# Kernel optimization log

Hardware: AMD Instinct MI355X
Metric: run time of the kernel (lower is better)

Reference implementation:

```python
import math
import jax, jax.numpy as jnp
import numpy as np
from jax import lax

MUL = 16           # multiplicity of 0e and 1o in input and output irreps
NRB = 8            # num_radial_basis
DIAMETER = 3.0
STEPS = (1.0, 1.0, 1.0)
DIM = 4 * MUL      # 16 scalars + 16 vectors * 3 = 64 channels


def _constants():
    # lattice from __init__: arange(-s, s+1) * step per axis, s = floor(r/step)
    r = DIAMETER / 2
    axes = [np.arange(-math.floor(r / st), math.floor(r / st) + 1.0) * st for st in STEPS]
    lattice = np.stack(np.meshgrid(*axes, indexing='ij'), axis=-1)  # [Kx,Ky,Kz,3]
    d = np.linalg.norm(lattice, axis=-1)                            # [Kx,Ky,Kz]
    # soft_one_hot_linspace(basis='smooth_finite', cutoff=True)
    values = np.linspace(0.0, r, NRB + 2)[1:-1]
    step = values[1] - values[0]
    diff = (d[..., None] - values) / step
    inside = diff ** 2 < 1.0
    emb = np.where(inside, 1.14136 * np.exp(2.0) * np.exp(-2.0 / np.where(inside, 1.0 - diff ** 2, 1.0)), 0.0)
    # spherical harmonics, normalize=True, normalization='component'
    n = lattice / np.maximum(d[..., None], 1e-12)  # unit vectors; 0 at the origin voxel
    sh0 = np.ones_like(d)                          # Y_0 (component normalized)
    sh1 = np.sqrt(3.0) * n                         # Y_1 (component normalized)
    return emb.astype(np.float32), sh0.astype(np.float32), sh1.astype(np.float32)

EMB, SH0, SH1 = _constants()
KX, KY, KZ = SH0.shape  # 3,3,3


def setup_inputs() -> dict:
    key = jax.random.key(0)
    ks = jax.random.split(key, 7)
    B, G = 4, 32
    return {
        'x': jax.random.normal(ks[0], (B, G, G, G, DIM), jnp.float32),
        'W_sc0': jax.random.normal(ks[1], (MUL, MUL), jnp.float32),  # Linear 0e->0e
        'W_sc1': jax.random.normal(ks[2], (MUL, MUL), jnp.float32),  # Linear 1o->1o
        'w1': jax.random.normal(ks[3], (NRB, MUL, MUL), jnp.float32),  # path 0e x 0e -> 0e
        'w2': jax.random.normal(ks[4], (NRB, MUL, MUL), jnp.float32),  # path 0e x 1o -> 1o
        'w3': jax.random.normal(ks[5], (NRB, MUL, MUL), jnp.float32),  # path 1o x 0e -> 1o
        'w4': jax.random.normal(ks[6], (NRB, MUL, MUL), jnp.float32),  # path 1o x 1o -> 0e
    }


def _kernel(w1, w2, w3, w4):
    # radial basis -> per-voxel path weights, divided by kernel volume (as in source)
    emb, sh0, sh1 = jnp.asarray(EMB), jnp.asarray(SH0), jnp.asarray(SH1)
    norm = float(KX * KY * KZ)
    W1, W2, W3, W4 = [jnp.einsum('xyzk,kio->xyzio', emb, w) / norm for w in (w1, w2, w3, w4)]
    # path normalization: each output irrep receives 2 paths of fan_in mul*1 = 16 -> 1/sqrt(32)
    alpha = 1.0 / np.sqrt(2.0 * MUL)
    # tp.right blocks (Clebsch-Gordan contractions, lmax=1):
    k00 = alpha * W1 * sh0[..., None, None]                                              # [.,i,o]
    k01 = alpha * jnp.einsum('xyzio,xyzm->xyziom', W2, sh1).reshape(KX, KY, KZ, MUL, 3 * MUL)
    k10 = (alpha / np.sqrt(3.0)) * jnp.einsum('xyzio,xyzm->xyzimo', W4, sh1).reshape(KX, KY, KZ, 3 * MUL, MUL)
    k11 = alpha * jnp.einsum('xyzio,mn->xyzimon', W3 * sh0[..., None, None],
                             jnp.eye(3, dtype=W3.dtype)).reshape(KX, KY, KZ, 3 * MUL, 3 * MUL)
    return jnp.concatenate([jnp.concatenate([k00, k01], axis=-1),
                            jnp.concatenate([k10, k11], axis=-1)], axis=-2)  # [Kx,Ky,Kz,64,64]


def reference(x, W_sc0, W_sc1, w1, w2, w3, w4):
    B, X, Y, Z, _ = x.shape
    inv_sqrt_mul = 1.0 / np.sqrt(MUL)
    # self-connection: e3nn Linear per irrep (applied pointwise over b,x,y,z)
    xs = x[..., :MUL]                                   # [B,X,Y,Z,16] scalars
    xv = x[..., MUL:].reshape(B, X, Y, Z, MUL, 3)       # [B,X,Y,Z,16,3] vectors
    sc_s = (xs @ W_sc0) * inv_sqrt_mul
    sc_v = jnp.einsum('bxyzic,io->bxyzoc', xv, W_sc1) * inv_sqrt_mul
    sc = jnp.concatenate([sc_s, sc_v.reshape(B, X, Y, Z, 3 * MUL)], axis=-1)
    # position-dependent equivariant kernel + standard 3D conv
    k = _kernel(w1, w2, w3, w4)
    conv = lax.conv_general_dilated(x, k, (1, 1, 1), 'SAME',
                                    dimension_numbers=('NXYZC', 'XYZIO', 'NXYZC'))
    return sc + conv
```

## Files before the change

kernel.cpp:

```cpp
#include <hip/hip_runtime.h>

typedef unsigned short u16;
typedef unsigned int u32;
typedef __bf16 bf16x8 __attribute__((ext_vector_type(8)));
typedef float f32x4 __attribute__((ext_vector_type(4)));
typedef u32 u32x4 __attribute__((ext_vector_type(4)));

#define AS1 __attribute__((address_space(1)))
#define AS3 __attribute__((address_space(3)))

__device__ __align__(16) u16 g_kT[27 * 64 * 64];
__device__ __align__(16) u16 g_kTr[27 * 8 * 512];

__device__ __forceinline__ u16 f2bf(float f) {
    unsigned int u = __float_as_uint(f);
    u += 0x7FFFu + ((u >> 16) & 1u);
    return (u16)(u >> 16);
}

__device__ __forceinline__ u32 pack_bf(float a, float b) {
    u32 ua = __float_as_uint(a) + 0x8000u;
    u32 ub = __float_as_uint(b) + 0x8000u;
    return __builtin_amdgcn_perm(ub, ua, 0x07060302u);
}

__global__ __launch_bounds__(64) void build_k(
    const float* __restrict__ Wsc0, const float* __restrict__ Wsc1,
    const float* __restrict__ w1, const float* __restrict__ w2,
    const float* __restrict__ w3, const float* __restrict__ w4)
{
    const int t = blockIdx.x;
    const int c = threadIdx.x;
    const int dx = t / 9 - 1, dy = (t / 3) % 3 - 1, dz = t % 3 - 1;
    const float d = sqrtf((float)(dx * dx + dy * dy + dz * dz));
    const float step = 1.5f / 9.0f;
    float emb[8];
#pragma unroll
    for (int k = 0; k < 8; ++k) {
        float diff = (d - (float)(k + 1) * step) / step;
        float q = diff * diff;
        emb[k] = (q < 1.0f) ? 1.14136f * expf(2.0f - 2.0f / (1.0f - q)) : 0.0f;
    }
    const float dn = fmaxf(d, 1e-12f);
    const float s3 = 1.7320508075688772f;
    const float sh1[3] = { s3 * (float)dx / dn, s3 * (float)dy / dn, s3 * (float)dz / dn };
    const float alpha  = 0.17677669529663687f;
    const float alpha3 = alpha * 0.57735026918962576f;

    u16* outp = &g_kT[(t * 64 + c) * 64];
    const int base2 = ((t * 2 + (c >> 5)) * 2 + ((c >> 4) & 1)) * 2;
    const int l15c  = c & 15;
    auto put = [&](int r, float v) {
        u16 h = f2bf(v);
        outp[r] = h;
        g_kTr[(base2 + (r >> 5)) * 512 + (((r >> 3) & 3) * 16 + l15c) * 8 + (r & 7)] = h;
    };

    if (c < 16) {
        const int o = c;
#pragma unroll
        for (int i = 0; i < 16; ++i) {
            float W1 = 0.f, W4 = 0.f;
#pragma unroll
            for (int k = 0; k < 8; ++k) {
                W1 += emb[k] * w1[k * 256 + i * 16 + o];
                W4 += emb[k] * w4[k * 256 + i * 16 + o];
            }
            W1 *= (1.0f / 27.0f); W4 *= (1.0f / 27.0f);
            float v0 = alpha * W1;
            if (t == 13) v0 += 0.25f * Wsc0[i * 16 + o];
            put(i, v0);
            const float base = alpha3 * W4;
#pragma unroll
            for (int m = 0; m < 3; ++m) put(16 + 3 * i + m, base * sh1[m]);
        }
    } else {
        const int o = (c - 16) / 3, nc = (c - 16) % 3;
#pragma unroll
        for (int i = 0; i < 16; ++i) {
            float W2 = 0.f, W3 = 0.f;
#pragma unroll
            for (int k = 0; k < 8; ++k) {
                W2 += emb[k] * w2[k * 256 + i * 16 + o];
                W3 += emb[k] * w3[k * 256 + i * 16 + o];
            }
            W2 *= (1.0f / 27.0f); W3 *= (1.0f / 27.0f);
            put(i, alpha * W2 * sh1[nc]);
#pragma unroll
            for (int m = 0; m < 3; ++m) {
                float v = (m == nc) ? alpha * W3 : 0.0f;
                if (t == 13 && m == nc) v += 0.25f * Wsc1[i * 16 + o];
                put(16 + 3 * i + m, v);
            }
        }
    }
}

__global__ __launch_bounds__(256) void cvt_x(
    const float* __restrict__ x, u16* __restrict__ xb, u32* __restrict__ zp)
{
    const int tid = threadIdx.x;
    if (blockIdx.x == 0) {
        u32x4 z = {0u, 0u, 0u, 0u};
        *reinterpret_cast<u32x4*>(zp + tid * 4) = z;
    }
    const size_t base = ((size_t)blockIdx.x * 256 + tid) * 8;
    const float4* s = reinterpret_cast<const float4*>(x + base);
    float4 v0 = s[0], v1 = s[1];
    u32x4 p;
    p[0] = pack_bf(v0.x, v0.y); p[1] = pack_bf(v0.z, v0.w);
    p[2] = pack_bf(v1.x, v1.y); p[3] = pack_bf(v1.z, v1.w);
    *reinterpret_cast<u32x4*>(xb + base) = p;
}

#define NROWS4 612
#define NCHUNK 77
#define LDSB   (NCHUNK * 1024)

#define ISSUE_B(s, t) \
  { const char* _p = bTr + (t) * 8192; \
    asm volatile("global_load_dwordx4 %0, %4, off\n\t" \
                 "global_load_dwordx4 %1, %4, off offset:1024\n\t" \
                 "global_load_dwordx4 %2, %4, off offset:2048\n\t" \
                 "global_load_dwordx4 %3, %4, off offset:3072" \
                 : "=&v"(B##s##0), "=&v"(B##s##1), "=&v"(B##s##2), "=&v"(B##s##3) \
                 : "v"(_p)); }

#define LOADA2(s, i0, i1, RCC) { \
  const int _r  = rbase + (RCC); \
  const int _o0 = _r * 128 + ((kg ^ (_r & 7)) << 4); \
  A##s##i0 = *reinterpret_cast<const bf16x8*>(abase + _o0); \
  A##s##i1 = *reinterpret_cast<const bf16x8*>(abase + (_o0 ^ 64)); }

#define RCC4(T, YY, MT) ((((T)/9)*6 + (YY) + (((T)/3)%3))*34 + ((T)%3) + (MT)*16)

#define LOAD_A8(s, T) \
  LOADA2(s, 0, 1, RCC4(T,0,0)) \
  LOADA2(s, 2, 3, RCC4(T,0,1)) \
  LOADA2(s, 4, 5, RCC4(T,1,0)) \
  LOADA2(s, 6, 7, RCC4(T,1,1))

#define WAITV(N) \
  asm volatile("s_waitcnt vmcnt(" #N ")" ::: "memory"); \
  __builtin_amdgcn_sched_barrier(0);

#define BC(x) __builtin_bit_cast(bf16x8, x)

#define MFMA16(bs, as) \
  acc000 = __builtin_amdgcn_mfma_f32_16x16x32_bf16(BC(B##bs##0), A##as##0, acc000, 0,0,0); \
  acc001 = __builtin_amdgcn_mfma_f32_16x16x32_bf16(BC(B##bs##2), A##as##0, acc001, 0,0,0); \
  acc010 = __builtin_amdgcn_mfma_f32_16x16x32_bf16(BC(B##bs##0), A##as##2, acc010, 0,0,0); \
  acc011 = __builtin_amdgcn_mfma_f32_16x16x32_bf16(BC(B##bs##2), A##as##2, acc011, 0,0,0); \
  acc100 = __builtin_amdgcn_mfma_f32_16x16x32_bf16(BC(B##bs##0), A##as##4, acc100, 0,0,0); \
  acc101 = __builtin_amdgcn_mfma_f32_16x16x32_bf16(BC(B##bs##2), A##as##4, acc101, 0,0,0); \
  acc110 = __builtin_amdgcn_mfma_f32_16x16x32_bf16(BC(B##bs##0), A##as##6, acc110, 0,0,0); \
  acc111 = __builtin_amdgcn_mfma_f32_16x16x32_bf16(BC(B##bs##2), A##as##6, acc111, 0,0,0); \
  acc000 = __builtin_amdgcn_mfma_f32_16x16x32_bf16(BC(B##bs##1), A##as##1, acc000, 0,0,0); \
  acc001 = __builtin_amdgcn_mfma_f32_16x16x32_bf16(BC(B##bs##3), A##as##1, acc001, 0,0,0); \
  acc010 = __builtin_amdgcn_mfma_f32_16x16x32_bf16(BC(B##bs##1), A##as##3, acc010, 0,0,0); \
  acc011 = __builtin_amdgcn_mfma_f32_16x16x32_bf16(BC(B##bs##3), A##as##3, acc011, 0,0,0); \
  acc100 = __builtin_amdgcn_mfma_f32_16x16x32_bf16(BC(B##bs##1), A##as##5, acc100, 0,0,0); \
  acc101 = __builtin_amdgcn_mfma_f32_16x16x32_bf16(BC(B##bs##3), A##as##5, acc101, 0,0,0); \
  acc110 = __builtin_amdgcn_mfma_f32_16x16x32_bf16(BC(B##bs##1), A##as##7, acc110, 0,0,0); \
  acc111 = __builtin_amdgcn_mfma_f32_16x16x32_bf16(BC(B##bs##3), A##as##7, acc111, 0,0,0);

__global__ __launch_bounds__(256, 2) void conv_mfma4(
    const u16* __restrict__ xb, const u32* __restrict__ zp,
    float* __restrict__ out)
{
    extern __shared__ u16 xt[];

    const int bid0 = blockIdx.x;
    const int bid  = (bid0 & 7) * 128 + (bid0 >> 3);
    const int b    = bid >> 8;
    const int X    = (bid >> 3) & 31;
    const int y0   = (bid & 7) << 2;
    const int tid  = threadIdx.x;
    const int wv   = tid >> 6;
    const int lane = tid & 63;
    const int l15  = lane & 15;
    const int kg   = lane >> 4;
    const int yh   = wv >> 1;
    const int nh   = wv & 1;

    const char* bTr = (const char*)g_kTr + nh * 4096 + lane * 16;

    u32x4 B00, B01, B02, B03, B10, B11, B12, B13, B20, B21, B22, B23;
    bf16x8 A00, A01, A02, A03, A04, A05, A06, A07;
    bf16x8 A10, A11, A12, A13, A14, A15, A16, A17;

    ISSUE_B(0, 1)
    ISSUE_B(1, 3)

    {
        const int rloc = lane >> 3;
        const int swz  = (lane & 7) ^ rloc;
#pragma unroll
        for (int i = 0; i < 20; ++i) {
            const int c = wv + i * 4;
            if (c < NCHUNK) {
                const int row = c * 8 + rloc;
                const int dxx = row / 204;
                const int rem = row - dxx * 204;
                const int yi  = rem / 34;
                const int zid = rem - yi * 34;
                const int xin = X + dxx - 1;
                const int yin = y0 + yi - 1;
                const int zin = zid - 1;
                const bool inb = (row < NROWS4) & ((unsigned)xin < 32u)
                               & ((unsigned)yin < 32u) & ((unsigned)zin < 32u);
                const u16* src = inb
                    ? xb + ((size_t)(((b * 32 + xin) * 32 + yin) * 32 + zin) * 64 + swz * 8)
                    : (const u16*)zp;
                __builtin_amdgcn_global_load_lds((const AS1 u32*)src,
                                                 (AS3 u32*)&xt[c * 512], 16, 0, 0);
            }
        }
    }
    asm volatile("s_waitcnt vmcnt(0)" ::: "memory");
    __syncthreads();

    const char* abase = reinterpret_cast<const char*>(xt);
    const int rbase = yh * 68 + l15;

    const f32x4 z4 = {0.f, 0.f, 0.f, 0.f};
    f32x4 acc000 = z4, acc001 = z4, acc010 = z4, acc011 = z4;
    f32x4 acc100 = z4, acc101 = z4, acc110 = z4, acc111 = z4;

    LOAD_A8(0, 1)

    ISSUE_B(2, 4)   LOAD_A8(1, 3)   WAITV(8)  MFMA16(0, 0)
    ISSUE_B(0, 5)   LOAD_A8(0, 4)   WAITV(8)  MFMA16(1, 1)
    ISSUE_B(1, 7)   LOAD_A8(1, 5)   WAITV(8)  MFMA16(2, 0)
    ISSUE_B(2, 9)   LOAD_A8(0, 7)   WAITV(8)  MFMA16(0, 1)
    ISSUE_B(0, 10)  LOAD_A8(1, 9)   WAITV(8)  MFMA16(1, 0)
    ISSUE_B(1, 11)  LOAD_A8(0, 10)  WAITV(8)  MFMA16(2, 1)
    ISSUE_B(2, 12)  LOAD_A8(1, 11)  WAITV(8)  MFMA16(0, 0)
    ISSUE_B(0, 13)  LOAD_A8(0, 12)  WAITV(8)  MFMA16(1, 1)
    ISSUE_B(1, 14)  LOAD_A8(1, 13)  WAITV(8)  MFMA16(2, 0)
    ISSUE_B(2, 15)  LOAD_A8(0, 14)  WAITV(8)  MFMA16(0, 1)
    ISSUE_B(0, 16)  LOAD_A8(1, 15)  WAITV(8)  MFMA16(1, 0)
    ISSUE_B(1, 17)  LOAD_A8(0, 16)  WAITV(8)  MFMA16(2, 1)
    ISSUE_B(2, 19)  LOAD_A8(1, 17)  WAITV(8)  MFMA16(0, 0)
    ISSUE_B(0, 21)  LOAD_A8(0, 19)  WAITV(8)  MFMA16(1, 1)
    ISSUE_B(1, 22)  LOAD_A8(1, 21)  WAITV(8)  MFMA16(2, 0)
    ISSUE_B(2, 23)  LOAD_A8(0, 22)  WAITV(8)  MFMA16(0, 1)
    ISSUE_B(0, 25)  LOAD_A8(1, 23)  WAITV(8)  MFMA16(1, 0)
                    LOAD_A8(0, 25)  WAITV(4)  MFMA16(2, 1)
                                    WAITV(0)  MFMA16(0, 0)

    float* obase = out + (((size_t)(b * 32 + X) * 32 + (y0 + yh * 2)) * 32) * 64
                 + nh * 32 + kg * 4;
    *reinterpret_cast<f32x4*>(obase + l15 * 64)               = acc000;
    *reinterpret_cast<f32x4*>(obase + l15 * 64 + 16)          = acc001;
    *reinterpret_cast<f32x4*>(obase + (16 + l15) * 64)        = acc010;
    *reinterpret_cast<f32x4*>(obase + (16 + l15) * 64 + 16)   = acc011;
    *reinterpret_cast<f32x4*>(obase + 2048 + l15 * 64)        = acc100;
    *reinterpret_cast<f32x4*>(obase + 2048 + l15 * 64 + 16)   = acc101;
    *reinterpret_cast<f32x4*>(obase + 2048 + (16 + l15) * 64) = acc110;
    *reinterpret_cast<f32x4*>(obase + 2048 + (16 + l15) * 64 + 16) = acc111;
}

#define ZS 68
#define NROWS 408

__global__ __launch_bounds__(256, 2) void conv_mfma_fb(
    const float* __restrict__ x, float* __restrict__ out)
{
    __shared__ __align__(16) u16 xts[NROWS * ZS];
    const int bid0 = blockIdx.x;
    const int bid  = (bid0 & 7) * 256 + (bid0 >> 3);
    const int b   = bid >> 9;
    const int X   = (bid >> 4) & 31;
    const int y0  = (bid & 15) << 1;
    const int tid = threadIdx.x;

    {
        const int pr = tid >> 2;
        const int q  = tid & 3;
#pragma unroll
        for (int pass = 0; pass < 7; ++pass) {
            const int idx = pass * 64 + pr;
            if (idx < NROWS) {
                const int rid = idx / 34;
                const int zid = idx - rid * 34;
                const int xin = X + (rid >> 2) - 1;
                const int yin = y0 + (rid & 3) - 1;
                const int zin = zid - 1;
                u32x4 p0 = {0u,0u,0u,0u}, p1 = {0u,0u,0u,0u};
                if ((unsigned)xin < 32u && (unsigned)yin < 32u && (unsigned)zin < 32u) {
                    const float4* src = reinterpret_cast<const float4*>(
                        x + ((((b * 32 + xin) * 32 + yin) * 32 + zin) * 64 + q * 16));
                    float4 v0 = src[0], v1 = src[1], v2 = src[2], v3 = src[3];
                    p0[0] = pack_bf(v0.x, v0.y); p0[1] = pack_bf(v0.z, v0.w);
                    p0[2] = pack_bf(v1.x, v1.y); p0[3] = pack_bf(v1.z, v1.w);
                    p1[0] = pack_bf(v2.x, v2.y); p1[1] = pack_bf(v2.z, v2.w);
                    p1[2] = pack_bf(v3.x, v3.y); p1[3] = pack_bf(v3.z, v3.w);
                }
                u16* dst = &xts[idx * ZS + q * 16];
                *reinterpret_cast<u32x4*>(dst)     = p0;
                *reinterpret_cast<u32x4*>(dst + 8) = p1;
            }
        }
    }
    __syncthreads();

    const int w    = tid >> 6;
    const int lane = tid & 63;
    const int l15  = lane & 15;
    const int kg   = lane >> 4;
    const int mh   = w >> 1;
    const int nh   = w & 1;
    const int chb  = kg * 8;

    const u16* abase = &xts[l15 * ZS + chb];
    const u16* bbase = &g_kT[(nh * 32 + l15) * 64 + chb];

    const f32x4 z4 = {0.f, 0.f, 0.f, 0.f};
    f32x4 acc[2][2] = {{z4, z4}, {z4, z4}};

    constexpr int NT = 19;
    constexpr int TAPS[NT] = {1,3,4,5,7,9,10,11,12,13,14,15,16,17,19,21,22,23,25};

#pragma unroll
    for (int ti = 0; ti < NT; ++ti) {
        const int t = TAPS[ti];
        const int dxt = t / 9, dyt = (t / 3) % 3, dzt = t % 3;
        const int rid = dxt * 4 + mh + dyt;
        bf16x8 bfr[4], afr[4];
#pragma unroll
        for (int kb = 0; kb < 2; ++kb)
#pragma unroll
        for (int nt = 0; nt < 2; ++nt)
            bfr[kb*2+nt] = *reinterpret_cast<const bf16x8*>(
                bbase + (t * 64 + nt * 16) * 64 + kb * 32);
#pragma unroll
        for (int kb = 0; kb < 2; ++kb)
#pragma unroll
        for (int mt = 0; mt < 2; ++mt)
            afr[kb*2+mt] = *reinterpret_cast<const bf16x8*>(
                abase + (rid * 34 + dzt + mt * 16) * ZS + kb * 32);
#pragma unroll
        for (int kb = 0; kb < 2; ++kb)
#pragma unroll
        for (int mt = 0; mt < 2; ++mt)
#pragma unroll
        for (int nt = 0; nt < 2; ++nt)
            acc[mt][nt] = __builtin_amdgcn_mfma_f32_16x16x32_bf16(
                bfr[kb*2+nt], afr[kb*2+mt], acc[mt][nt], 0, 0, 0);
    }

    float* obase = out + (((b * 32 + X) * 32 + (y0 + mh)) * 32) * 64 + nh * 32 + kg * 4;
#pragma unroll
    for (int mt = 0; mt < 2; ++mt)
#pragma unroll
        for (int nt = 0; nt < 2; ++nt) {
            float4 v;
            v.x = acc[mt][nt][0]; v.y = acc[mt][nt][1];
            v.z = acc[mt][nt][2]; v.w = acc[mt][nt][3];
            *reinterpret_cast<float4*>(obase + (mt * 16 + l15) * 64 + nt * 16) = v;
        }
}

extern "C" void kernel_launch(void* const* d_in, const int* in_sizes, int n_in,
                              void* d_out, int out_size, void* d_ws, size_t ws_size,
                              hipStream_t stream)
{
    const float* x    = (const float*)d_in[0];
    const float* Wsc0 = (const float*)d_in[1];
    const float* Wsc1 = (const float*)d_in[2];
    const float* w1   = (const float*)d_in[3];
    const float* w2   = (const float*)d_in[4];
    const float* w3   = (const float*)d_in[5];
    const float* w4   = (const float*)d_in[6];
    float* out = (float*)d_out;

    build_k<<<dim3(27), dim3(64), 0, stream>>>(Wsc0, Wsc1, w1, w2, w3, w4);

    const size_t xb_bytes = (size_t)4 * 32 * 32 * 32 * 64 * 2;
    if (ws_size >= 4096 + xb_bytes) {
        u32* zp = (u32*)d_ws;
        u16* xb = (u16*)((char*)d_ws + 4096);
        cvt_x<<<dim3(4096), dim3(256), 0, stream>>>(x, xb, zp);
        conv_mfma4<<<dim3(1024), dim3(256), LDSB, stream>>>(xb, zp, out);
    } else {
        conv_mfma_fb<<<dim3(2048), dim3(256), 0, stream>>>(x, out);
    }
}
```

Measured before the change: 56.78 us.

## Double per-block Y tile to 8 rows to cut halo reloads

The conv kernel now handles 8 y-rows per block instead of 4, so the LDS input tile grows to 10x34 rows per x-slice (128 KiB) and each wave keeps 16 accumulators instead of 8. The grid shrinks to 512 blocks and occupancy drops to one block per CU. The goal is to reuse each kernel-weight B fragment and each haloed input row over more outputs, which lowers global/L2 traffic and the share of halo loads. In exchange it raises register pressure, leaves fewer blocks than a 256-CU GPU can hold two of, and gives less latency hiding.

New measurement: 57.25 us. No clear change (+0.8%).

```diff
diff --git a/kernel.cpp b/kernel.cpp
--- a/kernel.cpp
+++ b/kernel.cpp
@@ -113,9 +113,9 @@
     *reinterpret_cast<u32x4*>(xb + base) = p;
 }
 
-#define NROWS4 612
-#define NCHUNK 77
-#define LDSB   (NCHUNK * 1024)
+#define NROWS5 1020
+#define NCHUNK5 128
+#define LDSB   (NCHUNK5 * 1024)
 
 #define ISSUE_B(s, t) \
   { const char* _p = bTr + (t) * 8192; \
@@ -129,52 +129,57 @@
 #define LOADA2(s, i0, i1, RCC) { \
   const int _r  = rbase + (RCC); \
   const int _o0 = _r * 128 + ((kg ^ (_r & 7)) << 4); \
-  A##s##i0 = *reinterpret_cast<const bf16x8*>(abase + _o0); \
-  A##s##i1 = *reinterpret_cast<const bf16x8*>(abase + (_o0 ^ 64)); }
-
-#define RCC4(T, YY, MT) ((((T)/9)*6 + (YY) + (((T)/3)%3))*34 + ((T)%3) + (MT)*16)
-
-#define LOAD_A8(s, T) \
-  LOADA2(s, 0, 1, RCC4(T,0,0)) \
-  LOADA2(s, 2, 3, RCC4(T,0,1)) \
-  LOADA2(s, 4, 5, RCC4(T,1,0)) \
-  LOADA2(s, 6, 7, RCC4(T,1,1))
+  A##s##_##i0 = *reinterpret_cast<const bf16x8*>(abase + _o0); \
+  A##s##_##i1 = *reinterpret_cast<const bf16x8*>(abase + (_o0 ^ 64)); }
+
+#define RCC5(T, YY, MT) ((((T)/9)*340 + ((((T)/3)%3) + (YY))*34 + ((T)%3) + (MT)*16))
+
+#define LOAD_A16(s, T) \
+  LOADA2(s, 0,  1,  RCC5(T,0,0)) \
+  LOADA2(s, 2,  3,  RCC5(T,0,1)) \
+  LOADA2(s, 4,  5,  RCC5(T,1,0)) \
+  LOADA2(s, 6,  7,  RCC5(T,1,1)) \
+  LOADA2(s, 8,  9,  RCC5(T,2,0)) \
+  LOADA2(s, 10, 11, RCC5(T,2,1)) \
+  LOADA2(s, 12, 13, RCC5(T,3,0)) \
+  LOADA2(s, 14, 15, RCC5(T,3,1))
 
 #define WAITV(N) \
   asm volatile("s_waitcnt vmcnt(" #N ")" ::: "memory"); \
   __builtin_amdgcn_sched_barrier(0);
 
 #define BC(x) __builtin_bit_cast(bf16x8, x)
-
-#define MFMA16(bs, as) \
-  acc000 = __builtin_amdgcn_mfma_f32_16x16x32_bf16(BC(B##bs##0), A##as##0, acc000, 0,0,0); \
-  acc001 = __builtin_amdgcn_mfma_f32_16x16x32_bf16(BC(B##bs##2), A##as##0, acc001, 0,0,0); \
-  acc010 = __builtin_amdgcn_mfma_f32_16x16x32_bf16(BC(B##bs##0), A##as##2, acc010, 0,0,0); \
-  acc011 = __builtin_amdgcn_mfma_f32_16x16x32_bf16(BC(B##bs##2), A##as##2, acc011, 0,0,0); \
-  acc100 = __builtin_amdgcn_mfma_f32_16x16x32_bf16(BC(B##bs##0), A##as##4, acc100, 0,0,0); \
-  acc101 = __builtin_amdgcn_mfma_f32_16x16x32_bf16(BC(B##bs##2), A##as##4, acc101, 0,0,0); \
-  acc110 = __builtin_amdgcn_mfma_f32_16x16x32_bf16(BC(B##bs##0), A##as##6, acc110, 0,0,0); \
-  acc111 = __builtin_amdgcn_mfma_f32_16x16x32_bf16(BC(B##bs##2), A##as##6, acc111, 0,0,0); \
-  acc000 = __builtin_amdgcn_mfma_f32_16x16x32_bf16(BC(B##bs##1), A##as##1, acc000, 0,0,0); \
-  acc001 = __builtin_amdgcn_mfma_f32_16x16x32_bf16(BC(B##bs##3), A##as##1, acc001, 0,0,0); \
-  acc010 = __builtin_amdgcn_mfma_f32_16x16x32_bf16(BC(B##bs##1), A##as##3, acc010, 0,0,0); \
-  acc011 = __builtin_amdgcn_mfma_f32_16x16x32_bf16(BC(B##bs##3), A##as##3, acc011, 0,0,0); \
-  acc100 = __builtin_amdgcn_mfma_f32_16x16x32_bf16(BC(B##bs##1), A##as##5, acc100, 0,0,0); \
-  acc101 = __builtin_amdgcn_mfma_f32_16x16x32_bf16(BC(B##bs##3), A##as##5, acc101, 0,0,0); \
-  acc110 = __builtin_amdgcn_mfma_f32_16x16x32_bf16(BC(B##bs##1), A##as##7, acc110, 0,0,0); \
-  acc111 = __builtin_amdgcn_mfma_f32_16x16x32_bf16(BC(B##bs##3), A##as##7, acc111, 0,0,0);
-
-__global__ __launch_bounds__(256, 2) void conv_mfma4(
+#define MF(b_, a_, c_) __builtin_amdgcn_mfma_f32_16x16x32_bf16(BC(b_), a_, c_, 0, 0, 0)
+
+#define MFMA32(bs, as) \
+  acc000 = MF(B##bs##0, A##as##_0,  acc000);  acc001 = MF(B##bs##2, A##as##_0,  acc001); \
+  acc010 = MF(B##bs##0, A##as##_2,  acc010);  acc011 = MF(B##bs##2, A##as##_2,  acc011); \
+  acc100 = MF(B##bs##0, A##as##_4,  acc100);  acc101 = MF(B##bs##2, A##as##_4,  acc101); \
+  acc110 = MF(B##bs##0, A##as##_6,  acc110);  acc111 = MF(B##bs##2, A##as##_6,  acc111); \
+  acc200 = MF(B##bs##0, A##as##_8,  acc200);  acc201 = MF(B##bs##2, A##as##_8,  acc201); \
+  acc210 = MF(B##bs##0, A##as##_10, acc210);  acc211 = MF(B##bs##2, A##as##_10, acc211); \
+  acc300 = MF(B##bs##0, A##as##_12, acc300);  acc301 = MF(B##bs##2, A##as##_12, acc301); \
+  acc310 = MF(B##bs##0, A##as##_14, acc310);  acc311 = MF(B##bs##2, A##as##_14, acc311); \
+  acc000 = MF(B##bs##1, A##as##_1,  acc000);  acc001 = MF(B##bs##3, A##as##_1,  acc001); \
+  acc010 = MF(B##bs##1, A##as##_3,  acc010);  acc011 = MF(B##bs##3, A##as##_3,  acc011); \
+  acc100 = MF(B##bs##1, A##as##_5,  acc100);  acc101 = MF(B##bs##3, A##as##_5,  acc101); \
+  acc110 = MF(B##bs##1, A##as##_7,  acc110);  acc111 = MF(B##bs##3, A##as##_7,  acc111); \
+  acc200 = MF(B##bs##1, A##as##_9,  acc200);  acc201 = MF(B##bs##3, A##as##_9,  acc201); \
+  acc210 = MF(B##bs##1, A##as##_11, acc210);  acc211 = MF(B##bs##3, A##as##_11, acc211); \
+  acc300 = MF(B##bs##1, A##as##_13, acc300);  acc301 = MF(B##bs##3, A##as##_13, acc301); \
+  acc310 = MF(B##bs##1, A##as##_15, acc310);  acc311 = MF(B##bs##3, A##as##_15, acc311);
+
+__global__ __launch_bounds__(256, 1) void conv_mfma5(
     const u16* __restrict__ xb, const u32* __restrict__ zp,
     float* __restrict__ out)
 {
     extern __shared__ u16 xt[];
 
     const int bid0 = blockIdx.x;
-    const int bid  = (bid0 & 7) * 128 + (bid0 >> 3);
-    const int b    = bid >> 8;
-    const int X    = (bid >> 3) & 31;
-    const int y0   = (bid & 7) << 2;
+    const int bid  = (bid0 & 7) * 64 + (bid0 >> 3);
+    const int b    = bid >> 7;
+    const int X    = (bid >> 2) & 31;
+    const int y0   = (bid & 3) << 3;
     const int tid  = threadIdx.x;
     const int wv   = tid >> 6;
     const int lane = tid & 63;
@@ -186,8 +191,10 @@
     const char* bTr = (const char*)g_kTr + nh * 4096 + lane * 16;
 
     u32x4 B00, B01, B02, B03, B10, B11, B12, B13, B20, B21, B22, B23;
-    bf16x8 A00, A01, A02, A03, A04, A05, A06, A07;
-    bf16x8 A10, A11, A12, A13, A14, A15, A16, A17;
+    bf16x8 A0_0, A0_1, A0_2,  A0_3,  A0_4,  A0_5,  A0_6,  A0_7,
+           A0_8, A0_9, A0_10, A0_11, A0_12, A0_13, A0_14, A0_15;
+    bf16x8 A1_0, A1_1, A1_2,  A1_3,  A1_4,  A1_5,  A1_6,  A1_7,
+           A1_8, A1_9, A1_10, A1_11, A1_12, A1_13, A1_14, A1_15;
 
     ISSUE_B(0, 1)
     ISSUE_B(1, 3)
@@ -196,69 +203,77 @@
         const int rloc = lane >> 3;
         const int swz  = (lane & 7) ^ rloc;
 #pragma unroll
-        for (int i = 0; i < 20; ++i) {
-            const int c = wv + i * 4;
-            if (c < NCHUNK) {
-                const int row = c * 8 + rloc;
-                const int dxx = row / 204;
-                const int rem = row - dxx * 204;
-                const int yi  = rem / 34;
-                const int zid = rem - yi * 34;
-                const int xin = X + dxx - 1;
-                const int yin = y0 + yi - 1;
-                const int zin = zid - 1;
-                const bool inb = (row < NROWS4) & ((unsigned)xin < 32u)
-                               & ((unsigned)yin < 32u) & ((unsigned)zin < 32u);
-                const u16* src = inb
-                    ? xb + ((size_t)(((b * 32 + xin) * 32 + yin) * 32 + zin) * 64 + swz * 8)
-                    : (const u16*)zp;
-                __builtin_amdgcn_global_load_lds((const AS1 u32*)src,
-                                                 (AS3 u32*)&xt[c * 512], 16, 0, 0);
-            }
+        for (int i = 0; i < 32; ++i) {
+            const int c = wv * 32 + i;
+            const int row = c * 8 + rloc;
+            const int dxx = row / 340;
+            const int rem = row - dxx * 340;
+            const int yi  = rem / 34;
+            const int zid = rem - yi * 34;
+            const int xin = X + dxx - 1;
+            const int yin = y0 + yi - 1;
+            const int zin = zid - 1;
+            const bool inb = (row < NROWS5) & ((unsigned)xin < 32u)
+                           & ((unsigned)yin < 32u) & ((unsigned)zin < 32u);
+            const u16* src = inb
+                ? xb + ((size_t)(((b * 32 + xin) * 32 + yin) * 32 + zin) * 64 + swz * 8)
+                : (const u16*)zp;
+            __builtin_amdgcn_global_load_lds((const AS1 u32*)src,
+                                             (AS3 u32*)&xt[c * 512], 16, 0, 0);
         }
     }
     asm volatile("s_waitcnt vmcnt(0)" ::: "memory");
     __syncthreads();
 
     const char* abase = reinterpret_cast<const char*>(xt);
-    const int rbase = yh * 68 + l15;
+    const int rbase = yh * 136 + l15;
 
     const f32x4 z4 = {0.f, 0.f, 0.f, 0.f};
     f32x4 acc000 = z4, acc001 = z4, acc010 = z4, acc011 = z4;
     f32x4 acc100 = z4, acc101 = z4, acc110 = z4, acc111 = z4;
-
-    LOAD_A8(0, 1)
-
-    ISSUE_B(2, 4)   LOAD_A8(1, 3)   WAITV(8)  MFMA16(0, 0)
-    ISSUE_B(0, 5)   LOAD_A8(0, 4)   WAITV(8)  MFMA16(1, 1)
-    ISSUE_B(1, 7)   LOAD_A8(1, 5)   WAITV(8)  MFMA16(2, 0)
-    ISSUE_B(2, 9)   LOAD_A8(0, 7)   WAITV(8)  MFMA16(0, 1)
-    ISSUE_B(0, 10)  LOAD_A8(1, 9)   WAITV(8)  MFMA16(1, 0)
-    ISSUE_B(1, 11)  LOAD_A8(0, 10)  WAITV(8)  MFMA16(2, 1)
-    ISSUE_B(2, 12)  LOAD_A8(1, 11)  WAITV(8)  MFMA16(0, 0)
-    ISSUE_B(0, 13)  LOAD_A8(0, 12)  WAITV(8)  MFMA16(1, 1)
-    ISSUE_B(1, 14)  LOAD_A8(1, 13)  WAITV(8)  MFMA16(2, 0)
-    ISSUE_B(2, 15)  LOAD_A8(0, 14)  WAITV(8)  MFMA16(0, 1)
-    ISSUE_B(0, 16)  LOAD_A8(1, 15)  WAITV(8)  MFMA16(1, 0)
-    ISSUE_B(1, 17)  LOAD_A8(0, 16)  WAITV(8)  MFMA16(2, 1)
-    ISSUE_B(2, 19)  LOAD_A8(1, 17)  WAITV(8)  MFMA16(0, 0)
-    ISSUE_B(0, 21)  LOAD_A8(0, 19)  WAITV(8)  MFMA16(1, 1)
-    ISSUE_B(1, 22)  LOAD_A8(1, 21)  WAITV(8)  MFMA16(2, 0)
-    ISSUE_B(2, 23)  LOAD_A8(0, 22)  WAITV(8)  MFMA16(0, 1)
-    ISSUE_B(0, 25)  LOAD_A8(1, 23)  WAITV(8)  MFMA16(1, 0)
-                    LOAD_A8(0, 25)  WAITV(4)  MFMA16(2, 1)
-                                    WAITV(0)  MFMA16(0, 0)
-
-    float* obase = out + (((size_t)(b * 32 + X) * 32 + (y0 + yh * 2)) * 32) * 64
+    f32x4 acc200 = z4, acc201 = z4, acc210 = z4, acc211 = z4;
+    f32x4 acc300 = z4, acc301 = z4, acc310 = z4, acc311 = z4;
+
+    LOAD_A16(0, 1)
+
+    ISSUE_B(2, 4)   LOAD_A16(1, 3)   WAITV(8)  MFMA32(0, 0)
+    ISSUE_B(0, 5)   LOAD_A16(0, 4)   WAITV(8)  MFMA32(1, 1)
+    ISSUE_B(1, 7)   LOAD_A16(1, 5)   WAITV(8)  MFMA32(2, 0)
+    ISSUE_B(2, 9)   LOAD_A16(0, 7)   WAITV(8)  MFMA32(0, 1)
+    ISSUE_B(0, 10)  LOAD_A16(1, 9)   WAITV(8)  MFMA32(1, 0)
+    ISSUE_B(1, 11)  LOAD_A16(0, 10)  WAITV(8)  MFMA32(2, 1)
+    ISSUE_B(2, 12)  LOAD_A16(1, 11)  WAITV(8)  MFMA32(0, 0)
+    ISSUE_B(0, 13)  LOAD_A16(0, 12)  WAITV(8)  MFMA32(1, 1)
+    ISSUE_B(1, 14)  LOAD_A16(1, 13)  WAITV(8)  MFMA32(2, 0)
+    ISSUE_B(2, 15)  LOAD_A16(0, 14)  WAITV(8)  MFMA32(0, 1)
+    ISSUE_B(0, 16)  LOAD_A16(1, 15)  WAITV(8)  MFMA32(1, 0)
+    ISSUE_B(1, 17)  LOAD_A16(0, 16)  WAITV(8)  MFMA32(2, 1)
+    ISSUE_B(2, 19)  LOAD_A16(1, 17)  WAITV(8)  MFMA32(0, 0)
+    ISSUE_B(0, 21)  LOAD_A16(0, 19)  WAITV(8)  MFMA32(1, 1)
+    ISSUE_B(1, 22)  LOAD_A16(1, 21)  WAITV(8)  MFMA32(2, 0)
+    ISSUE_B(2, 23)  LOAD_A16(0, 22)  WAITV(8)  MFMA32(0, 1)
+    ISSUE_B(0, 25)  LOAD_A16(1, 23)  WAITV(8)  MFMA32(1, 0)
+                    LOAD_A16(0, 25)  WAITV(4)  MFMA32(2, 1)
+                                     WAITV(0)  MFMA32(0, 0)
+
+    float* obase = out + (((size_t)(b * 32 + X) * 32 + (y0 + yh * 4)) * 32) * 64
                  + nh * 32 + kg * 4;
-    *reinterpret_cast<f32x4*>(obase + l15 * 64)               = acc000;
-    *reinterpret_cast<f32x4*>(obase + l15 * 64 + 16)          = acc001;
-    *reinterpret_cast<f32x4*>(obase + (16 + l15) * 64)        = acc010;
-    *reinterpret_cast<f32x4*>(obase + (16 + l15) * 64 + 16)   = acc011;
-    *reinterpret_cast<f32x4*>(obase + 2048 + l15 * 64)        = acc100;
-    *reinterpret_cast<f32x4*>(obase + 2048 + l15 * 64 + 16)   = acc101;
-    *reinterpret_cast<f32x4*>(obase + 2048 + (16 + l15) * 64) = acc110;
+    *reinterpret_cast<f32x4*>(obase + l15 * 64)                    = acc000;
+    *reinterpret_cast<f32x4*>(obase + l15 * 64 + 16)               = acc001;
+    *reinterpret_cast<f32x4*>(obase + (16 + l15) * 64)             = acc010;
+    *reinterpret_cast<f32x4*>(obase + (16 + l15) * 64 + 16)        = acc011;
+    *reinterpret_cast<f32x4*>(obase + 2048 + l15 * 64)             = acc100;
+    *reinterpret_cast<f32x4*>(obase + 2048 + l15 * 64 + 16)        = acc101;
+    *reinterpret_cast<f32x4*>(obase + 2048 + (16 + l15) * 64)      = acc110;
     *reinterpret_cast<f32x4*>(obase + 2048 + (16 + l15) * 64 + 16) = acc111;
+    *reinterpret_cast<f32x4*>(obase + 4096 + l15 * 64)             = acc200;
+    *reinterpret_cast<f32x4*>(obase + 4096 + l15 * 64 + 16)        = acc201;
+    *reinterpret_cast<f32x4*>(obase + 4096 + (16 + l15) * 64)      = acc210;
+    *reinterpret_cast<f32x4*>(obase + 4096 + (16 + l15) * 64 + 16) = acc211;
+    *reinterpret_cast<f32x4*>(obase + 6144 + l15 * 64)             = acc300;
+    *reinterpret_cast<f32x4*>(obase + 6144 + l15 * 64 + 16)        = acc301;
+    *reinterpret_cast<f32x4*>(obase + 6144 + (16 + l15) * 64)      = acc310;
+    *reinterpret_cast<f32x4*>(obase + 6144 + (16 + l15) * 64 + 16) = acc311;
 }
 
 #define ZS 68
@@ -382,7 +397,7 @@
         u32* zp = (u32*)d_ws;
         u16* xb = (u16*)((char*)d_ws + 4096);
         cvt_x<<<dim3(4096), dim3(256), 0, stream>>>(x, xb, zp);
-        conv_mfma4<<<dim3(1024), dim3(256), LDSB, stream>>>(xb, zp, out);
+        conv_mfma5<<<dim3(512), dim3(256), LDSB, stream>>>(xb, zp, out);
     } else {
         conv_mfma_fb<<<dim3(2048), dim3(256), 0, stream>>>(x, out);
     }
```
